# Optimization experiments

Hardware: AMD Instinct MI355X
Metric: run time of the kernel (lower is better)

Reference implementation:

```python
import jax, jax.numpy as jnp
import numpy as np
from jax import lax

SR = 16000
N_FFT = 400
HOP = 200
N_MELS = 128
HID = 128


def _mel_fb():
    # torchaudio melscale_fbanks defaults: htk scale, norm=None, f_min=0, f_max=sr/2
    all_freqs = np.linspace(0.0, SR / 2, N_FFT // 2 + 1)  # (201,)
    hz2mel = lambda f: 2595.0 * np.log10(1.0 + f / 700.0)
    mel2hz = lambda m: 700.0 * (10.0 ** (m / 2595.0) - 1.0)
    m_pts = np.linspace(hz2mel(0.0), hz2mel(SR / 2), N_MELS + 2)
    f_pts = mel2hz(m_pts)  # (130,)
    f_diff = np.diff(f_pts)  # (129,)
    slopes = f_pts[None, :] - all_freqs[:, None]  # (201,130)
    down = -slopes[:, :-2] / f_diff[:-1]
    up = slopes[:, 2:] / f_diff[1:]
    fb = np.maximum(0.0, np.minimum(down, up))  # (201,128)
    return jnp.asarray(fb, dtype=jnp.float32)

MEL_FB = _mel_fb()
HANN = jnp.asarray(np.hanning(N_FFT + 1)[:-1], dtype=jnp.float32)  # periodic hann(400)


def mel_spectrogram(x):
    # x: (B, T) waveform -> (B, n_mels, frames), power=2 mel spectrogram
    pad = N_FFT // 2
    xp = jnp.pad(x, ((0, 0), (pad, pad)), mode='reflect')
    n_frames = 1 + (xp.shape[1] - N_FFT) // HOP  # 81 for T=16000
    idx = jnp.arange(n_frames)[:, None] * HOP + jnp.arange(N_FFT)[None, :]
    frames = xp[:, idx] * HANN  # (B, frames, 400)
    spec = jnp.fft.rfft(frames, axis=-1)  # (B, frames, 201)
    power = jnp.abs(spec) ** 2
    mel = power @ MEL_FB  # (B, frames, 128)
    return jnp.transpose(mel, (0, 2, 1))  # (B, 128, frames)


def lstm_layer(x, W, U, b):
    # x: (B, T, F); gate order i, f, g, o (matches torch slicing)
    B = x.shape[0]
    h0 = jnp.zeros((B, HID), x.dtype)
    c0 = jnp.zeros((B, HID), x.dtype)

    def step(carry, x_t):
        h, c = carry
        gates = x_t @ W + h @ U + b  # (B, 4H)
        i = jax.nn.sigmoid(gates[:, :HID])
        f = jax.nn.sigmoid(gates[:, HID:2 * HID])
        g = jnp.tanh(gates[:, 2 * HID:3 * HID])
        o = jax.nn.sigmoid(gates[:, 3 * HID:])
        c = f * c + i * g
        h = o * jnp.tanh(c)
        return (h, c), h

    _, hs = lax.scan(step, (h0, c0), jnp.transpose(x, (1, 0, 2)))  # (T, B, H)
    return jnp.transpose(hs, (1, 0, 2))  # (B, T, H)


def setup_inputs() -> dict:
    key = jax.random.key(0)
    ks = jax.random.split(key, 16)
    s = 0.05
    return {
        'x': jax.random.normal(ks[0], (1024, 16000), dtype=jnp.float32),
        'conv_w': jax.random.normal(ks[1], (128, 128, 3), dtype=jnp.float32) * s,  # (out,in,k)
        'conv_b': jax.random.normal(ks[2], (128,), dtype=jnp.float32) * s,
        'W1': jax.random.normal(ks[3], (128, 4 * HID), dtype=jnp.float32) * s,
        'U1': jax.random.normal(ks[4], (HID, 4 * HID), dtype=jnp.float32) * s,
        'b1': jax.random.normal(ks[5], (4 * HID,), dtype=jnp.float32) * s,
        'W2': jax.random.normal(ks[6], (HID, 4 * HID), dtype=jnp.float32) * s,
        'U2': jax.random.normal(ks[7], (HID, 4 * HID), dtype=jnp.float32) * s,
        'b2': jax.random.normal(ks[8], (4 * HID,), dtype=jnp.float32) * s,
        'fc1_w': jax.random.normal(ks[9], (128, 128), dtype=jnp.float32) * s,  # (in,out)
        'fc1_b': jax.random.normal(ks[10], (128,), dtype=jnp.float32) * s,
        'proj_w': jax.random.normal(ks[11], (128, 35), dtype=jnp.float32) * s,  # (in,out)
        'proj_b': jax.random.normal(ks[12], (35,), dtype=jnp.float32) * s,
    }


def reference(x, conv_w, conv_b, W1, U1, b1, W2, U2, b2, fc1_w, fc1_b, proj_w, proj_b):
    # MelSpectrogram -> Conv1d(128,128,3) -> permute -> LSTM x2 -> fc1 -> mean(time) -> proj
    spec = mel_spectrogram(x)  # (B, 128, 81)
    conv = lax.conv_general_dilated(
        spec, conv_w, window_strides=(1,), padding='VALID',
        dimension_numbers=('NCH', 'OIH', 'NCH')) + conv_b[None, :, None]  # (B,128,79)
    h = jnp.transpose(conv, (0, 2, 1))  # (B, 79, 128)
    h = lstm_layer(h, W1, U1, b1)
    h = lstm_layer(h, W2, U2, b2)
    h = h @ fc1_w + fc1_b  # (B, 79, 128)
    h = jnp.mean(h, axis=1)  # (B, 128)
    return h @ proj_w + proj_b  # (B, 35)
```

## Files before the change

kernel.cpp:

```cpp
#include <hip/hip_runtime.h>
#include <math.h>

#define PI_D 3.14159265358979323846

#define BATCH   1024
#define TLEN    16000
#define NFFT    400
#define HOP     200
#define NFRAME  81
#define NBIN    201
#define NMEL    128
#define HID     128
#define TSTEPS  79
#define GATES   512

#define KDFT    416
#define NDFT    512
#define SINOFF  256
#define KPOW    224
#define KCONV   384
#define NCHUNK  2
#define CHROWS  (BATCH*NFRAME/NCHUNK)

static inline size_t al512(size_t v){ return (v + 511) & ~((size_t)511); }

__device__ __forceinline__ unsigned short bf_rne(float f){
    unsigned u = __float_as_uint(f);
    u += 0x7FFF + ((u >> 16) & 1);
    return (unsigned short)(u >> 16);
}
__device__ __forceinline__ void bf_split(float f, unsigned short& h, unsigned short& l){
    h = bf_rne(f);
    float hf = __uint_as_float(((unsigned)h) << 16);
    l = bf_rne(f - hf);
}
__device__ __forceinline__ void bf_split_fast(float f, unsigned short& h, unsigned short& l){
    unsigned u = __float_as_uint(f);
    h = (unsigned short)(u >> 16);
    float hf = __uint_as_float(u & 0xFFFF0000u);
    l = (unsigned short)(__float_as_uint(f - hf) >> 16);
}

typedef short bf16x8 __attribute__((ext_vector_type(8)));
typedef float f32x4  __attribute__((ext_vector_type(4)));
typedef unsigned short us8 __attribute__((ext_vector_type(8)));
typedef unsigned short us4 __attribute__((ext_vector_type(4)));
typedef _Float16 f16x8 __attribute__((ext_vector_type(8)));

__global__ void setup_dft_t(unsigned short* __restrict__ th, unsigned short* __restrict__ tl){
    int idx = blockIdx.x*256 + threadIdx.x;
    if (idx >= NDFT*KDFT) return;
    int n = idx / KDFT, k = idx % KDFT;
    double v = 0.0;
    if (k < 400) {
        double w = 0.5 - 0.5*cos(2.0*PI_D*(double)k/400.0);
        if (n < NBIN)                              v = w * cos(2.0*PI_D*(double)((k*n)%400)/400.0);
        else if (n >= SINOFF && n < SINOFF + NBIN) v = w * sin(2.0*PI_D*(double)((k*(n-SINOFF))%400)/400.0);
    }
    unsigned short h, l; bf_split((float)v, h, l);
    th[idx] = h; tl[idx] = l;
}

__global__ void setup_fb_t(unsigned short* __restrict__ fh, unsigned short* __restrict__ fl){
    int idx = blockIdx.x*256 + threadIdx.x;
    if (idx >= NMEL*KPOW) return;
    int m = idx / KPOW, f = idx % KPOW;
    float v = 0.f;
    if (f < NBIN) {
        double melmax = 2595.0 * log10(1.0 + 8000.0/700.0);
        double p0 = 700.0*(pow(10.0, melmax*(double)(m  )/129.0/2595.0) - 1.0);
        double p1 = 700.0*(pow(10.0, melmax*(double)(m+1)/129.0/2595.0) - 1.0);
        double p2 = 700.0*(pow(10.0, melmax*(double)(m+2)/129.0/2595.0) - 1.0);
        double freq = 40.0 * (double)f;
        double dn = (freq - p0)/(p1 - p0);
        double up = (p2 - freq)/(p2 - p1);
        double t  = dn < up ? dn : up;
        if (t < 0.0) t = 0.0;
        v = (float)t;
    }
    unsigned short h, l; bf_split(v, h, l);
    fh[idx] = h; fl[idx] = l;
}

__global__ void setup_wc_t(unsigned short* __restrict__ wh, unsigned short* __restrict__ wl,
                           const float* __restrict__ cw){
    int idx = blockIdx.x*256 + threadIdx.x;
    if (idx >= NMEL*KCONV) return;
    int o = idx / KCONV, kk = idx % KCONV;
    int ksh = kk >> 7, i = kk & 127;
    unsigned short h, l; bf_split(cw[o*384 + i*3 + ksh], h, l);
    wh[idx] = h; wl[idx] = l;
}

__global__ void setup_w_t(unsigned short* __restrict__ wh, unsigned short* __restrict__ wl,
                          const float* __restrict__ w){
    int idx = blockIdx.x*256 + threadIdx.x;
    if (idx >= GATES*HID) return;
    int c = idx / HID, i = idx % HID;
    unsigned short h, l; bf_split(w[(size_t)i*GATES + c], h, l);
    wh[idx] = h; wl[idx] = l;
}

__global__ void setup_comb(float* __restrict__ cwm, float* __restrict__ cb,
                           const float* __restrict__ fc1w, const float* __restrict__ fc1b,
                           const float* __restrict__ projw, const float* __restrict__ projb){
    int idx = blockIdx.x*256 + threadIdx.x;
    if (idx < 128*64) {
        int i = idx / 64, o = idx % 64;
        float v = 0.f;
        if (o < 35) {
            double s = 0.0;
            for (int m = 0; m < 128; m++) s += (double)fc1w[i*128+m] * (double)projw[m*35+o];
            v = (float)s;
        }
        cwm[idx] = v;
    } else if (idx < 128*64 + 64) {
        int o = idx - 128*64;
        float v = 0.f;
        if (o < 35) {
            double s = (double)projb[o];
            for (int m = 0; m < 128; m++) s += (double)fc1b[m] * (double)projw[m*35+o];
            v = (float)s;
        }
        cb[o] = v;
    }
}

__global__ void setup_uf(_Float16* __restrict__ uf, const float* __restrict__ u){
    int idx = blockIdx.x*256 + threadIdx.x;
    if (idx >= 65536) return;
    int j    = idx & 7;
    int lane = (idx >> 3) & 63;
    int nt   = (idx >> 9) & 3;
    int ks   = (idx >> 11) & 3;
    int w    = (idx >> 13) & 7;
    int k = ks*32 + (lane >> 4)*8 + j;
    int c = w*64 + nt*16 + (lane & 15);
    uf[idx] = (_Float16)u[(size_t)k*GATES + c];
}

enum AMode { A_NORMAL=0, A_FRAMES=1, A_POWER=2, A_CONV3=3 };
#define LDK 40

template<int AMODE, bool BIAS, int NT>
__global__ __launch_bounds__(256)
void mgemm_k(const float* __restrict__ A,
             const unsigned short* __restrict__ BTh, const unsigned short* __restrict__ BTl,
             const float* __restrict__ bias, float* __restrict__ C,
             int Ksteps, int lda, int kstride, int ldc,
             const float* __restrict__ aux, int rowbase)
{
    __shared__ unsigned short Ash[128][LDK], Asl[128][LDK];
    __shared__ unsigned short Bsh[128][LDK], Bsl[128][LDK];

    const int nwg = gridDim.x;
    const int qq = nwg >> 3, rmd = nwg & 7;
    const int xcd = blockIdx.x & 7, loc = blockIdx.x >> 3;
    const int swz = (xcd < rmd ? xcd*(qq+1) : rmd*(qq+1) + (xcd - rmd)*qq) + loc;
    constexpr int LGNT = (NT == 4) ? 2 : 0;
    const int m0 = (swz >> LGNT) * 128;
    const int n0 = (swz & (NT-1)) * 128;

    const int tid = threadIdx.x;
    const int sr = tid >> 3;
    const int sk = (tid & 7) * 4;
    const int br = tid >> 2;
    const int bk = (tid & 3) * 8;

    const int lane = tid & 63, w = tid >> 6;
    const int wr = (w >> 1) * 64, wc = (w & 1) * 64;
    const int l15 = lane & 15, koff = (lane >> 4) * 8;

    f32x4 acc[4][4] = {};

    for (int ks = 0; ks < Ksteps; ks++) {
        const int k0 = ks * 32;
        #pragma unroll
        for (int p = 0; p < 4; p++) {
            const int row = p*32 + sr;
            const int kk = k0 + sk;
            float v[4];
            if constexpr (AMODE == A_NORMAL) {
                *(float4*)v = *(const float4*)(A + (size_t)(m0+row)*lda + kk);
            } else if constexpr (AMODE == A_POWER) {
                const float* src = A + (size_t)(m0+row)*lda + kk;
                float4 re = *(const float4*)(src);
                float4 im = *(const float4*)(src + SINOFF);
                v[0]=re.x*re.x+im.x*im.x; v[1]=re.y*re.y+im.y*im.y;
                v[2]=re.z*re.z+im.z*im.z; v[3]=re.w*re.w+im.w*im.w;
            } else if constexpr (AMODE == A_FRAMES) {
                const int rr = rowbase + m0 + row;
                const int b = rr / NFRAME, f = rr - b*NFRAME;
                const float* xb = aux + (size_t)b * TLEN;
                const int q0 = f*HOP + kk - 200;
                if (q0 >= 0 && q0 + 3 < TLEN) {
                    *(float4*)v = *(const float4*)(xb + q0);
                } else {
                    #pragma unroll
                    for (int j = 0; j < 4; j++) {
                        int q = q0 + j;
                        if (q < 0) q = -q;
                        else if (q >= TLEN) q = 2*TLEN - 2 - q;
                        v[j] = xb[q];
                    }
                }
            } else {
                const int rr = m0 + row;
                const int b = rr / TSTEPS, t = rr - b*TSTEPS;
                const int ksh = kk >> 7, i = kk & 127;
                *(float4*)v = *(const float4*)(aux + ((size_t)(b*NFRAME + t + ksh)*NMEL + i));
            }
            us4 hv, lv;
            #pragma unroll
            for (int j = 0; j < 4; j++) {
                unsigned short h, l; bf_split_fast(v[j], h, l);
                hv[j] = h; lv[j] = l;
            }
            *(us4*)&Ash[row][sk] = hv;
            *(us4*)&Asl[row][sk] = lv;
        }
        #pragma unroll
        for (int p = 0; p < 2; p++) {
            const int row = p*64 + br;
            const size_t o = (size_t)(n0 + row)*kstride + k0 + bk;
            *(us8*)&Bsh[row][bk] = *(const us8*)(BTh + o);
            *(us8*)&Bsl[row][bk] = *(const us8*)(BTl + o);
        }
        __syncthreads();

        bf16x8 ah[4], al[4];
        #pragma unroll
        for (int mt = 0; mt < 4; mt++) {
            ah[mt] = *(const bf16x8*)&Ash[wr + mt*16 + l15][koff];
            al[mt] = *(const bf16x8*)&Asl[wr + mt*16 + l15][koff];
        }
        #pragma unroll
        for (int nt = 0; nt < 4; nt++) {
            const int nr = wc + nt*16 + l15;
            bf16x8 bh = *(const bf16x8*)&Bsh[nr][koff];
            bf16x8 bl = *(const bf16x8*)&Bsl[nr][koff];
            #pragma unroll
            for (int mt = 0; mt < 4; mt++) {
                acc[mt][nt] = __builtin_amdgcn_mfma_f32_16x16x32_bf16(ah[mt], bh, acc[mt][nt], 0, 0, 0);
                acc[mt][nt] = __builtin_amdgcn_mfma_f32_16x16x32_bf16(ah[mt], bl, acc[mt][nt], 0, 0, 0);
                acc[mt][nt] = __builtin_amdgcn_mfma_f32_16x16x32_bf16(al[mt], bh, acc[mt][nt], 0, 0, 0);
            }
        }
        __syncthreads();
    }

    const int quad = lane >> 4;
    #pragma unroll
    for (int nt = 0; nt < 4; nt++) {
        const int col = n0 + wc + (nt << 4) + l15;
        float b = 0.f;
        if constexpr (BIAS) b = bias[col];
        #pragma unroll
        for (int mt = 0; mt < 4; mt++) {
            #pragma unroll
            for (int r = 0; r < 4; r++) {
                const int row = m0 + wr + (mt << 4) + quad*4 + r;
                C[(size_t)row*ldc + col] = acc[mt][nt][r] + b;
            }
        }
    }
}

__global__ __launch_bounds__(256)
void gemm_small(const float* __restrict__ A, const float* __restrict__ Bm,
                const float* __restrict__ bias, float* __restrict__ C,
                int M, int N, int K, int lda, int ldb, int ldc)
{
    __shared__ float As[16][64+4];
    __shared__ float Bs[16][64];
    const int tid = threadIdx.x;
    const int tx = tid & 15, ty = tid >> 4;
    const int m0 = blockIdx.x * 64;
    float acc[4][4] = {{0,0,0,0},{0,0,0,0},{0,0,0,0},{0,0,0,0}};
    const int am = tid >> 2, ak = (tid & 3) * 4;
    const int bk = tid >> 4, bn = (tid & 15) * 4;
    for (int k0 = 0; k0 < K; k0 += 16) {
        float4 av = *(const float4*)(A + (size_t)(m0+am)*lda + k0 + ak);
        As[ak+0][am]=av.x; As[ak+1][am]=av.y; As[ak+2][am]=av.z; As[ak+3][am]=av.w;
        *(float4*)&Bs[bk][bn] = *(const float4*)(Bm + (size_t)(k0+bk)*ldb + bn);
        __syncthreads();
        #pragma unroll
        for (int k = 0; k < 16; k++) {
            float4 a = *(const float4*)&As[k][ty*4];
            float4 b = *(const float4*)&Bs[k][tx*4];
            #pragma unroll
            for (int i = 0; i < 4; i++) {
                float av_ = ((const float*)&a)[i];
                acc[i][0] = fmaf(av_, b.x, acc[i][0]);
                acc[i][1] = fmaf(av_, b.y, acc[i][1]);
                acc[i][2] = fmaf(av_, b.z, acc[i][2]);
                acc[i][3] = fmaf(av_, b.w, acc[i][3]);
            }
        }
        __syncthreads();
    }
    #pragma unroll
    for (int ir = 0; ir < 4; ir++) {
        const int row = m0 + ty*4 + ir;
        #pragma unroll
        for (int jc = 0; jc < 4; jc++) {
            const int col = tx*4 + jc;
            if (col < N) C[(size_t)row*ldc + col] = acc[ir][jc] + bias[col];
        }
    }
}

__device__ __forceinline__ float sigm_f(float x){ return 1.f/(1.f + __expf(-x)); }
__device__ __forceinline__ float tanh_f(float x){ float e = __expf(2.f*x); return 1.f - 2.f/(e + 1.f); }

#define LROWS 4
#define LTHREADS 512
#define HPAD 136

__global__ __launch_bounds__(LTHREADS, 2)
void lstm_k(const float* __restrict__ X, const _Float16* __restrict__ Uf, float* __restrict__ H)
{
    __shared__ _Float16 hsA[16*HPAD];
    __shared__ float gs[GATES*5];
    const int tid = threadIdx.x;
    const int b0 = blockIdx.x * LROWS;
    const int lane = tid & 63, w = tid >> 6;
    const int m16 = lane & 15, quad = lane >> 4;
    const int r = tid >> 7;
    const int j = tid & 127;

    f32x4 bfr[4][4];
    #pragma unroll
    for (int ks = 0; ks < 4; ks++)
        #pragma unroll
        for (int nt = 0; nt < 4; nt++) {
            bfr[ks][nt] = *(const f32x4*)(Uf + ((((w*4 + ks)*4 + nt)*64 + lane) << 3));
            asm volatile("" : "+v"(bfr[ks][nt]));
        }

    for (int i = tid; i < 16*HPAD; i += LTHREADS) hsA[i] = (_Float16)0.f;
    float cst = 0.f;
    const float* xb = X + ((size_t)(b0 + r)*TSTEPS)*GATES + j;
    __syncthreads();

    float xi = xb[0], xf = xb[128], xg = xb[256], xo = xb[384];

    for (int t = 0; t < TSTEPS; t++) {
        float xi_n = 0.f, xf_n = 0.f, xg_n = 0.f, xo_n = 0.f;
        if (t + 1 < TSTEPS) {
            const float* xp = xb + (size_t)(t + 1)*GATES;
            xi_n = xp[0]; xf_n = xp[128]; xg_n = xp[256]; xo_n = xp[384];
        }

        f16x8 ah[4];
        #pragma unroll
        for (int ks = 0; ks < 4; ks++)
            ah[ks] = *(const f16x8*)&hsA[m16*HPAD + ks*32 + quad*8];

        f32x4 acc[4] = {{0,0,0,0},{0,0,0,0},{0,0,0,0},{0,0,0,0}};
        #pragma unroll
        for (int ks = 0; ks < 4; ks++)
            #pragma unroll
            for (int nt = 0; nt < 4; nt++)
                acc[nt] = __builtin_amdgcn_mfma_f32_16x16x32_f16(
                    ah[ks], __builtin_bit_cast(f16x8, bfr[ks][nt]), acc[nt], 0, 0, 0);

        if (quad == 0) {
            #pragma unroll
            for (int nt = 0; nt < 4; nt++) {
                const int c = w*64 + nt*16 + m16;
                #pragma unroll
                for (int rr = 0; rr < 4; rr++) gs[c*5 + rr] = acc[nt][rr];
            }
        }
        __syncthreads();

        {
            const float gi = gs[(      j)*5 + r] + xi;
            const float gf = gs[(128 + j)*5 + r] + xf;
            const float gg = gs[(256 + j)*5 + r] + xg;
            const float go = gs[(384 + j)*5 + r] + xo;
            const float cn = sigm_f(gf)*cst + sigm_f(gi)*tanh_f(gg);
            cst = cn;
            const float hn = sigm_f(go)*tanh_f(cn);
            H[((size_t)(b0 + r)*TSTEPS + t)*HID + j] = hn;
            hsA[r*HPAD + j] = (_Float16)hn;
        }
        __syncthreads();

        xi = xi_n; xf = xf_n; xg = xg_n; xo = xo_n;
    }
}

__global__ void mean_k(const float* __restrict__ H, float* __restrict__ Mh){
    const int idx = blockIdx.x*256 + threadIdx.x;
    if (idx >= BATCH*HID) return;
    const int b = idx >> 7, j = idx & 127;
    const float* p = H + (size_t)b*TSTEPS*HID + j;
    float s = 0.f;
    for (int t = 0; t < TSTEPS; t++) s += p[(size_t)t*HID];
    Mh[idx] = s * (1.0f/(float)TSTEPS);
}

extern "C" void kernel_launch(void* const* d_in, const int* in_sizes, int n_in,
                              void* d_out, int out_size, void* d_ws, size_t ws_size,
                              hipStream_t stream)
{
    const float* x      = (const float*)d_in[0];
    const float* conv_w = (const float*)d_in[1];
    const float* conv_b = (const float*)d_in[2];
    const float* W1     = (const float*)d_in[3];
    const float* U1     = (const float*)d_in[4];
    const float* b1     = (const float*)d_in[5];
    const float* W2     = (const float*)d_in[6];
    const float* U2     = (const float*)d_in[7];
    const float* b2     = (const float*)d_in[8];
    const float* fc1_w  = (const float*)d_in[9];
    const float* fc1_b  = (const float*)d_in[10];
    const float* proj_w = (const float*)d_in[11];
    const float* proj_b = (const float*)d_in[12];
    float* out = (float*)d_out;

    char* ws = (char*)d_ws;
    size_t off = 0;
    unsigned short* Tth = (unsigned short*)(ws + off); off = al512(off + (size_t)NDFT*KDFT*2);
    unsigned short* Ttl = (unsigned short*)(ws + off); off = al512(off + (size_t)NDFT*KDFT*2);
    unsigned short* fbh = (unsigned short*)(ws + off); off = al512(off + (size_t)NMEL*KPOW*2);
    unsigned short* fbl = (unsigned short*)(ws + off); off = al512(off + (size_t)NMEL*KPOW*2);
    unsigned short* wch = (unsigned short*)(ws + off); off = al512(off + (size_t)NMEL*KCONV*2);
    unsigned short* wcl = (unsigned short*)(ws + off); off = al512(off + (size_t)NMEL*KCONV*2);
    unsigned short* w1h = (unsigned short*)(ws + off); off = al512(off + (size_t)GATES*HID*2);
    unsigned short* w1l = (unsigned short*)(ws + off); off = al512(off + (size_t)GATES*HID*2);
    unsigned short* w2h = (unsigned short*)(ws + off); off = al512(off + (size_t)GATES*HID*2);
    unsigned short* w2l = (unsigned short*)(ws + off); off = al512(off + (size_t)GATES*HID*2);
    float* Cw   = (float*)(ws + off); off = al512(off + (size_t)128*64*4);
    float* Cb   = (float*)(ws + off); off = al512(off + (size_t)64*4);
    float* Mh   = (float*)(ws + off); off = al512(off + (size_t)BATCH*HID*4);
    _Float16* Uf1 = (_Float16*)(ws + off); off = al512(off + (size_t)65536*2);
    _Float16* Uf2 = (_Float16*)(ws + off); off = al512(off + (size_t)65536*2);
    float* MEL  = (float*)(ws + off); off = al512(off + (size_t)BATCH*NFRAME*NMEL*4);
    float* CONV = (float*)(ws + off); off = al512(off + (size_t)BATCH*TSTEPS*NMEL*4);
    float* X    = (float*)(ws + off); off = al512(off + (size_t)BATCH*TSTEPS*GATES*4);
    float* DFT = X;
    float* H1  = MEL;
    float* H2  = CONV;
    (void)ws_size; (void)out_size; (void)n_in; (void)in_sizes;

    setup_dft_t<<<(NDFT*KDFT + 255)/256, 256, 0, stream>>>(Tth, Ttl);
    setup_fb_t <<<(NMEL*KPOW + 255)/256, 256, 0, stream>>>(fbh, fbl);
    setup_wc_t <<<(NMEL*KCONV + 255)/256, 256, 0, stream>>>(wch, wcl, conv_w);
    setup_w_t  <<<(GATES*HID + 255)/256, 256, 0, stream>>>(w1h, w1l, W1);
    setup_w_t  <<<(GATES*HID + 255)/256, 256, 0, stream>>>(w2h, w2l, W2);
    setup_comb <<<(128*64 + 64 + 255)/256, 256, 0, stream>>>(Cw, Cb, fc1_w, fc1_b, proj_w, proj_b);
    setup_uf   <<<65536/256, 256, 0, stream>>>(Uf1, U1);
    setup_uf   <<<65536/256, 256, 0, stream>>>(Uf2, U2);

    for (int ch = 0; ch < NCHUNK; ch++) {
        const int rowbase = ch * CHROWS;
        mgemm_k<A_FRAMES,false,4><<<(CHROWS/128)*4, 256, 0, stream>>>(
            nullptr, Tth, Ttl, nullptr, DFT, KDFT/32, 0, KDFT, NDFT, x, rowbase);
        mgemm_k<A_POWER,false,1><<<CHROWS/128, 256, 0, stream>>>(
            DFT, fbh, fbl, nullptr, MEL + (size_t)rowbase*NMEL, KPOW/32, NDFT, KPOW, NMEL, nullptr, 0);
    }

    mgemm_k<A_CONV3,true,1><<<BATCH*TSTEPS/128, 256, 0, stream>>>(
        nullptr, wch, wcl, conv_b, CONV, KCONV/32, 0, KCONV, NMEL, MEL, 0);

    mgemm_k<A_NORMAL,true,4><<<(BATCH*TSTEPS/128)*4, 256, 0, stream>>>(
        CONV, w1h, w1l, b1, X, HID/32, NMEL, HID, GATES, nullptr, 0);
    lstm_k<<<BATCH/LROWS, LTHREADS, 0, stream>>>(X, Uf1, H1);

    mgemm_k<A_NORMAL,true,4><<<(BATCH*TSTEPS/128)*4, 256, 0, stream>>>(
        H1, w2h, w2l, b2, X, HID/32, HID, HID, GATES, nullptr, 0);
    lstm_k<<<BATCH/LROWS, LTHREADS, 0, stream>>>(X, Uf2, H2);

    mean_k<<<(BATCH*HID + 255)/256, 256, 0, stream>>>(H2, Mh);
    gemm_small<<<BATCH/64, 256, 0, stream>>>(Mh, Cw, Cb, out, BATCH, 35, HID, HID, 64, 35);
}
```

Baseline: 689.1 us.

## Double-buffer GEMM LDS tiles with direct-to-LDS B loads and XOR swizzle

Measured after the change: 688.3 us. Within noise of the previous version (-0.1%).

```diff
diff --git a/kernel.cpp b/kernel.cpp
--- a/kernel.cpp
+++ b/kernel.cpp
@@ -41,11 +41,21 @@
     l = (unsigned short)(__float_as_uint(f - hf) >> 16);
 }
 
+__device__ __forceinline__ int kswz(int n, int k){
+    return (k & ~31) | (((((k >> 3) & 3) ^ ((n >> 1) & 3))) << 3) | (k & 7);
+}
+
 typedef short bf16x8 __attribute__((ext_vector_type(8)));
 typedef float f32x4  __attribute__((ext_vector_type(4)));
 typedef unsigned short us8 __attribute__((ext_vector_type(8)));
 typedef unsigned short us4 __attribute__((ext_vector_type(4)));
 typedef _Float16 f16x8 __attribute__((ext_vector_type(8)));
+
+__device__ __forceinline__ void gld16(const unsigned short* g, unsigned short* l){
+    __builtin_amdgcn_global_load_lds(
+        (const __attribute__((address_space(1))) unsigned int*)g,
+        (__attribute__((address_space(3))) unsigned int*)l, 16, 0, 0);
+}
 
 __global__ void setup_dft_t(unsigned short* __restrict__ th, unsigned short* __restrict__ tl){
     int idx = blockIdx.x*256 + threadIdx.x;
@@ -58,7 +68,8 @@
         else if (n >= SINOFF && n < SINOFF + NBIN) v = w * sin(2.0*PI_D*(double)((k*(n-SINOFF))%400)/400.0);
     }
     unsigned short h, l; bf_split((float)v, h, l);
-    th[idx] = h; tl[idx] = l;
+    int o = n*KDFT + kswz(n, k);
+    th[o] = h; tl[o] = l;
 }
 
 __global__ void setup_fb_t(unsigned short* __restrict__ fh, unsigned short* __restrict__ fl){
@@ -79,7 +90,8 @@
         v = (float)t;
     }
     unsigned short h, l; bf_split(v, h, l);
-    fh[idx] = h; fl[idx] = l;
+    int o = m*KPOW + kswz(m, f);
+    fh[o] = h; fl[o] = l;
 }
 
 __global__ void setup_wc_t(unsigned short* __restrict__ wh, unsigned short* __restrict__ wl,
@@ -89,7 +101,8 @@
     int o = idx / KCONV, kk = idx % KCONV;
     int ksh = kk >> 7, i = kk & 127;
     unsigned short h, l; bf_split(cw[o*384 + i*3 + ksh], h, l);
-    wh[idx] = h; wl[idx] = l;
+    int p = o*KCONV + kswz(o, kk);
+    wh[p] = h; wl[p] = l;
 }
 
 __global__ void setup_w_t(unsigned short* __restrict__ wh, unsigned short* __restrict__ wl,
@@ -98,7 +111,8 @@
     if (idx >= GATES*HID) return;
     int c = idx / HID, i = idx % HID;
     unsigned short h, l; bf_split(w[(size_t)i*GATES + c], h, l);
-    wh[idx] = h; wl[idx] = l;
+    int p = c*HID + kswz(c, i);
+    wh[p] = h; wl[p] = l;
 }
 
 __global__ void setup_comb(float* __restrict__ cwm, float* __restrict__ cb,
@@ -140,7 +154,6 @@
 }
 
 enum AMode { A_NORMAL=0, A_FRAMES=1, A_POWER=2, A_CONV3=3 };
-#define LDK 40
 
 template<int AMODE, bool BIAS, int NT>
 __global__ __launch_bounds__(256)
@@ -150,8 +163,8 @@
              int Ksteps, int lda, int kstride, int ldc,
              const float* __restrict__ aux, int rowbase)
 {
-    __shared__ unsigned short Ash[128][LDK], Asl[128][LDK];
-    __shared__ unsigned short Bsh[128][LDK], Bsl[128][LDK];
+    __shared__ unsigned short Ash[2][128][32], Asl[2][128][32];
+    __shared__ unsigned short Bsh[2][128][32], Bsl[2][128][32];
 
     const int nwg = gridDim.x;
     const int qq = nwg >> 3, rmd = nwg & 7;
@@ -162,83 +175,105 @@
     const int n0 = (swz & (NT-1)) * 128;
 
     const int tid = threadIdx.x;
-    const int sr = tid >> 3;
-    const int sk = (tid & 7) * 4;
-    const int br = tid >> 2;
-    const int bk = (tid & 3) * 8;
-
     const int lane = tid & 63, w = tid >> 6;
     const int wr = (w >> 1) * 64, wc = (w & 1) * 64;
-    const int l15 = lane & 15, koff = (lane >> 4) * 8;
-
-    f32x4 acc[4][4] = {};
-
-    for (int ks = 0; ks < Ksteps; ks++) {
-        const int k0 = ks * 32;
+    const int l15 = lane & 15;
+    const int swf = ((lane & 15) >> 1) & 3;
+    const int pos = (((lane >> 4) ^ swf) << 3);
+
+    const int sr  = tid >> 3;
+    const int wcol = (((((tid & 7) >> 1)) ^ ((tid >> 4) & 3)) << 3) + ((tid & 1) << 2);
+
+    float va[16], vb[16];
+
+    auto issue_loads = [&](int ksn){
+        const int k0n = ksn * 32;
         #pragma unroll
         for (int p = 0; p < 4; p++) {
             const int row = p*32 + sr;
-            const int kk = k0 + sk;
-            float v[4];
+            const int kk = k0n + (tid & 7)*4;
             if constexpr (AMODE == A_NORMAL) {
-                *(float4*)v = *(const float4*)(A + (size_t)(m0+row)*lda + kk);
+                *(float4*)&va[p*4] = *(const float4*)(A + (size_t)(m0+row)*lda + kk);
             } else if constexpr (AMODE == A_POWER) {
                 const float* src = A + (size_t)(m0+row)*lda + kk;
-                float4 re = *(const float4*)(src);
-                float4 im = *(const float4*)(src + SINOFF);
-                v[0]=re.x*re.x+im.x*im.x; v[1]=re.y*re.y+im.y*im.y;
-                v[2]=re.z*re.z+im.z*im.z; v[3]=re.w*re.w+im.w*im.w;
+                *(float4*)&va[p*4] = *(const float4*)(src);
+                *(float4*)&vb[p*4] = *(const float4*)(src + SINOFF);
             } else if constexpr (AMODE == A_FRAMES) {
                 const int rr = rowbase + m0 + row;
                 const int b = rr / NFRAME, f = rr - b*NFRAME;
                 const float* xb = aux + (size_t)b * TLEN;
                 const int q0 = f*HOP + kk - 200;
                 if (q0 >= 0 && q0 + 3 < TLEN) {
-                    *(float4*)v = *(const float4*)(xb + q0);
+                    *(float4*)&va[p*4] = *(const float4*)(xb + q0);
                 } else {
                     #pragma unroll
                     for (int j = 0; j < 4; j++) {
                         int q = q0 + j;
                         if (q < 0) q = -q;
                         else if (q >= TLEN) q = 2*TLEN - 2 - q;
-                        v[j] = xb[q];
+                        va[p*4+j] = xb[q];
                     }
                 }
             } else {
                 const int rr = m0 + row;
                 const int b = rr / TSTEPS, t = rr - b*TSTEPS;
                 const int ksh = kk >> 7, i = kk & 127;
-                *(float4*)v = *(const float4*)(aux + ((size_t)(b*NFRAME + t + ksh)*NMEL + i));
+                *(float4*)&va[p*4] = *(const float4*)(aux + ((size_t)(b*NFRAME + t + ksh)*NMEL + i));
             }
+        }
+    };
+    auto write_stage = [&](int wb){
+        #pragma unroll
+        for (int p = 0; p < 4; p++) {
+            const int row = p*32 + sr;
             us4 hv, lv;
             #pragma unroll
             for (int j = 0; j < 4; j++) {
-                unsigned short h, l; bf_split_fast(v[j], h, l);
+                float f = va[p*4+j];
+                if constexpr (AMODE == A_POWER) f = f*f + vb[p*4+j]*vb[p*4+j];
+                unsigned short h, l; bf_split_fast(f, h, l);
                 hv[j] = h; lv[j] = l;
             }
-            *(us4*)&Ash[row][sk] = hv;
-            *(us4*)&Asl[row][sk] = lv;
-        }
+            *(us4*)&Ash[wb][row][wcol] = hv;
+            *(us4*)&Asl[wb][row][wcol] = lv;
+        }
+    };
+    auto dma_b = [&](int wb, int ksn){
+        const int k0n = ksn * 32;
         #pragma unroll
         for (int p = 0; p < 2; p++) {
-            const int row = p*64 + br;
-            const size_t o = (size_t)(n0 + row)*kstride + k0 + bk;
-            *(us8*)&Bsh[row][bk] = *(const us8*)(BTh + o);
-            *(us8*)&Bsl[row][bk] = *(const us8*)(BTl + o);
-        }
-        __syncthreads();
+            const size_t o = (size_t)(n0 + p*64 + w*16 + (lane >> 2))*kstride + k0n + (lane & 3)*8;
+            gld16(BTh + o, &Bsh[wb][p*64 + w*16][0]);
+            gld16(BTl + o, &Bsl[wb][p*64 + w*16][0]);
+        }
+    };
+
+    f32x4 acc[4][4] = {};
+
+    issue_loads(0);
+    dma_b(0, 0);
+    write_stage(0);
+    __syncthreads();
+
+    int buf = 0;
+    for (int ks = 0; ks < Ksteps; ks++) {
+        const bool pf = (ks + 1 < Ksteps);
+        if (pf) {
+            dma_b(buf ^ 1, ks + 1);
+            issue_loads(ks + 1);
+        }
 
         bf16x8 ah[4], al[4];
         #pragma unroll
         for (int mt = 0; mt < 4; mt++) {
-            ah[mt] = *(const bf16x8*)&Ash[wr + mt*16 + l15][koff];
-            al[mt] = *(const bf16x8*)&Asl[wr + mt*16 + l15][koff];
+            ah[mt] = *(const bf16x8*)&Ash[buf][wr + mt*16 + l15][pos];
+            al[mt] = *(const bf16x8*)&Asl[buf][wr + mt*16 + l15][pos];
         }
         #pragma unroll
         for (int nt = 0; nt < 4; nt++) {
             const int nr = wc + nt*16 + l15;
-            bf16x8 bh = *(const bf16x8*)&Bsh[nr][koff];
-            bf16x8 bl = *(const bf16x8*)&Bsl[nr][koff];
+            bf16x8 bh = *(const bf16x8*)&Bsh[buf][nr][pos];
+            bf16x8 bl = *(const bf16x8*)&Bsl[buf][nr][pos];
             #pragma unroll
             for (int mt = 0; mt < 4; mt++) {
                 acc[mt][nt] = __builtin_amdgcn_mfma_f32_16x16x32_bf16(ah[mt], bh, acc[mt][nt], 0, 0, 0);
@@ -246,7 +281,12 @@
                 acc[mt][nt] = __builtin_amdgcn_mfma_f32_16x16x32_bf16(al[mt], bh, acc[mt][nt], 0, 0, 0);
             }
         }
-        __syncthreads();
+
+        if (pf) {
+            write_stage(buf ^ 1);
+            __syncthreads();
+        }
+        buf ^= 1;
     }
 
     const int quad = lane >> 4;
```
